# Kernel optimization log

Hardware: AMD Instinct MI355X
Metric: run time of the kernel (lower is better)

The kernel has to match this reference:

```python
import math
import jax, jax.numpy as jnp
import numpy as np

B, T, C, H = 2, 2048, 1024, 16
MAX_SEQ = 2048


def _make_pe(max_seq: int, dim: int, base: float = 10000.0) -> np.ndarray:
    pe = np.zeros((max_seq, dim), dtype=np.float32)
    position = np.arange(max_seq, dtype=np.float32)[:, None]
    div_term = np.exp(np.arange(0, dim, 2, dtype=np.float32) * (-math.log(base) / dim))
    pe[:, 0::2] = np.sin(position * div_term)
    pe[:, 1::2] = np.cos(position * div_term)
    return pe


def setup_inputs() -> dict:
    key = jax.random.key(0)
    k1, k2, k3 = jax.random.split(key, 3)
    x = jax.random.normal(k1, (B, T, C), dtype=jnp.float32)
    # torch Linear default init scale ~ 1/sqrt(fan_in)
    w_qkv = jax.random.normal(k2, (3 * C, C), dtype=jnp.float32) / math.sqrt(C)
    w_proj = jax.random.normal(k3, (C, C), dtype=jnp.float32) / math.sqrt(C)
    pe = jnp.asarray(_make_pe(MAX_SEQ, C))
    return {"x": x, "w_qkv": w_qkv, "w_proj": w_proj, "pe": pe}


def reference(x, w_qkv, w_proj, pe):
    b, t, c = x.shape
    h = H
    d = c // h
    # RoPE module adds sinusoidal PE under torch.no_grad() -> stop_gradient
    xp = jax.lax.stop_gradient(x + pe[None, :t, :])
    qkv = xp @ w_qkv.T  # [b, t, 3c]
    q, k, v = jnp.split(qkv, 3, axis=-1)
    q = q.reshape(b, t, h, d).transpose(0, 2, 1, 3)  # bhtd
    k = k.reshape(b, t, h, d).transpose(0, 2, 1, 3)
    v = v.reshape(b, t, h, d).transpose(0, 2, 1, 3)
    att = jnp.einsum("bhqd,bhkd->bhqk", q, k) * (1.0 / math.sqrt(d))
    causal = jnp.tril(jnp.ones((t, t), dtype=bool))  # [t, t]
    att = jnp.where(causal[None, None], att, -jnp.inf)
    att = jax.nn.softmax(att, axis=-1)
    y = jnp.einsum("bhqk,bhkd->bhqd", att, v)
    y = y.transpose(0, 2, 1, 3).reshape(b, t, c)
    return y @ w_proj.T
```

## Files before the change

kernel.cpp:

```cpp
#include <hip/hip_runtime.h>
#include <cstdint>

typedef __bf16 bf16x8 __attribute__((ext_vector_type(8)));
typedef __bf16 bf16x4 __attribute__((ext_vector_type(4)));
typedef float  f32x4  __attribute__((ext_vector_type(4)));

static constexpr int kB = 2, kT = 2048, kC = 1024, kH = 16, kD = 64;
static constexpr int kK = 1024;

__device__ __forceinline__ uint16_t f2bf(float f) {
  uint32_t u = __builtin_bit_cast(uint32_t, f);
  u += 0x7FFFu + ((u >> 16) & 1u);
  return (uint16_t)(u >> 16);
}

__device__ __forceinline__ void gl_lds16(const void* g, void* l) {
  __builtin_amdgcn_global_load_lds((__attribute__((address_space(1))) void*)(void*)g,
                                   (__attribute__((address_space(3))) void*)l, 16, 0, 0);
}

__global__ __launch_bounds__(256) void prep_xpe(const float* __restrict__ x,
                                                const float* __restrict__ pe,
                                                uint16_t* __restrict__ xp) {
  const int i = blockIdx.x * 256 + threadIdx.x;
  const float4 xv = ((const float4*)x)[i];
  const int c4 = i & (kC / 4 - 1);
  const int t = (i / (kC / 4)) & (kT - 1);
  const float4 pv = ((const float4*)pe)[t * (kC / 4) + c4];
  ushort4 o;
  o.x = f2bf(xv.x + pv.x);
  o.y = f2bf(xv.y + pv.y);
  o.z = f2bf(xv.z + pv.z);
  o.w = f2bf(xv.w + pv.w);
  ((ushort4*)xp)[i] = o;
}

__global__ __launch_bounds__(256) void cast_w(const float* __restrict__ w,
                                              uint16_t* __restrict__ o) {
  const int i = blockIdx.x * 256 + threadIdx.x;
  const float4 v = ((const float4*)w)[i];
  ushort4 u;
  u.x = f2bf(v.x); u.y = f2bf(v.y); u.z = f2bf(v.z); u.w = f2bf(v.w);
  ((ushort4*)o)[i] = u;
}

__global__ __launch_bounds__(512, 2) void gemm_qkv(const uint16_t* __restrict__ A,
                                                   const uint16_t* __restrict__ W,
                                                   uint16_t* __restrict__ qb,
                                                   uint16_t* __restrict__ kb,
                                                   uint16_t* __restrict__ vT) {
  __shared__ __align__(1024) char lds[131072];
  const int tid = threadIdx.x;
  const int lane = tid & 63;
  const int wid = tid >> 6;
  const int l15 = lane & 15, l4 = lane >> 4;
  const int WM = wid >> 2, WN = wid & 3;
  const int orig = (int)blockIdx.x;
  const int xcd = orig & 7, j = orig >> 3;
  const int m0 = (xcd * 2 + (j & 1)) * 256;
  const int n0 = (j >> 1) * 256;
  constexpr int NKT = kK / 64;
  constexpr int NIT = NKT / 2;

  f32x4 acc[4][4][2] = {};

  auto stage = [&](int isA, int buf, int half, int kt) {
#pragma unroll
    for (int c = 0; c < 2; ++c) {
      const int off = (c * 512 + tid) * 16;
      const int lr = off >> 7, cbl = off & 127;
      const size_t grow = (size_t)((isA ? m0 : n0) + half * 128 + lr) * kK + kt * 64;
      gl_lds16((const char*)(isA ? A : W) + grow * 2 + (cbl ^ ((lr & 7) << 4)),
               lds + (isA ? 0 : 65536) + buf * 32768 + half * 16384 + off);
    }
  };
  auto bar = [&] {
    asm volatile("" ::: "memory");
    __builtin_amdgcn_s_barrier();
    asm volatile("" ::: "memory");
  };

  stage(1, 0, 0, 0); stage(0, 0, 0, 0);
  stage(1, 0, 1, 0); stage(0, 0, 1, 0);
  stage(1, 1, 0, 1); stage(0, 1, 0, 1);

  for (int i = 0; i < NIT; ++i) {
#pragma unroll
    for (int p = 0; p < 8; ++p) {
      constexpr int ISA[8] = {1, 0, 1, 0, 1, 0, 1, 0};
      constexpr int HLF[8] = {1, 1, 0, 0, 1, 1, 0, 0};
      constexpr int TOF[8] = {1, 1, 2, 2, 2, 2, 3, 3};
      const int qr = (p >> 1) & 1, qc = p & 1;
      const int cbuf = (p >> 2) & 1, q4 = p & 3;
      {
        int kt = 2 * i + TOF[p];
        if (kt > NKT - 1) kt = NKT - 1;
        stage(ISA[p], TOF[p] & 1, HLF[p], kt);
      }
      const char* Ab = lds + cbuf * 32768 + qr * 16384;
      const char* Bb = lds + 65536 + cbuf * 32768 + qc * 16384;
      bf16x8 af[2][4], bfr[2][2];
      auto reads = [&] {
#pragma unroll
        for (int ks = 0; ks < 2; ++ks) {
#pragma unroll
          for (int mt = 0; mt < 4; ++mt) {
            const int lr = WM * 64 + mt * 16 + l15;
            af[ks][mt] = *(const bf16x8*)(Ab + lr * 128 +
                                          ((ks * 64 + l4 * 16) ^ ((lr & 7) << 4)));
          }
#pragma unroll
          for (int nt = 0; nt < 2; ++nt) {
            const int lr = WN * 32 + nt * 16 + l15;
            bfr[ks][nt] = *(const bf16x8*)(Bb + lr * 128 +
                                           ((ks * 64 + l4 * 16) ^ ((lr & 7) << 4)));
          }
        }
      };
      if (p == 0 || p == 4) {
        asm volatile("s_waitcnt vmcnt(6)" ::: "memory");
        bar();
        reads();
      } else {
        reads();
        bar();
      }
      __builtin_amdgcn_s_setprio(1);
#pragma unroll
      for (int ks = 0; ks < 2; ++ks)
#pragma unroll
        for (int mt = 0; mt < 4; ++mt)
#pragma unroll
          for (int nt = 0; nt < 2; ++nt)
            acc[q4][mt][nt] = __builtin_amdgcn_mfma_f32_16x16x32_bf16(
                af[ks][mt], bfr[ks][nt], acc[q4][mt][nt], 0, 0, 0);
      __builtin_amdgcn_s_setprio(0);
      bar();
    }
  }
  asm volatile("s_waitcnt vmcnt(0)" ::: "memory");
  bar();

  const int sec = n0 >> 10;
  const int b = m0 >> 11, tb = m0 & (kT - 1);
  if (sec < 2) {
    uint16_t* dst = (sec == 0) ? qb : kb;
#pragma unroll
    for (int q4 = 0; q4 < 4; ++q4) {
      const int qr = q4 >> 1, qc = q4 & 1;
#pragma unroll
      for (int mt = 0; mt < 4; ++mt)
#pragma unroll
        for (int nt = 0; nt < 2; ++nt)
#pragma unroll
          for (int r = 0; r < 4; ++r) {
            const int m = qr * 128 + WM * 64 + mt * 16 + l4 * 4 + r;
            const int nn = (n0 & (kC - 1)) + qc * 128 + WN * 32 + nt * 16 + l15;
            const int h = nn >> 6, d = nn & 63;
            dst[((size_t)((b * kH + h) * kT + tb + m)) * kD + d] =
                f2bf(acc[q4][mt][nt][r]);
          }
    }
  } else {
#pragma unroll
    for (int q4 = 0; q4 < 4; ++q4) {
      const int qr = q4 >> 1, qc = q4 & 1;
#pragma unroll
      for (int mt = 0; mt < 4; ++mt)
#pragma unroll
        for (int nt = 0; nt < 2; ++nt) {
          const int nl = qc * 128 + WN * 32 + nt * 16 + l15;
          const int mb2 = (qr * 128 + WM * 64 + mt * 16 + l4 * 4) * 2;
          ushort4 pk;
          pk.x = f2bf(acc[q4][mt][nt][0]);
          pk.y = f2bf(acc[q4][mt][nt][1]);
          pk.z = f2bf(acc[q4][mt][nt][2]);
          pk.w = f2bf(acc[q4][mt][nt][3]);
          *(ushort4*)(lds + nl * 512 + (mb2 ^ ((nl & 7) << 4))) = pk;
        }
    }
    bar();
#pragma unroll
    for (int it = 0; it < 16; ++it) {
      const int chunk = it * 512 + tid;
      const int nr = chunk >> 5, mb = (chunk & 31) * 16;
      const bf16x8 v = *(const bf16x8*)(lds + nr * 512 + (mb ^ ((nr & 7) << 4)));
      const int nn = (n0 - 2048) + nr;
      const int h = nn >> 6, d = nn & 63;
      *(bf16x8*)(vT + ((size_t)((b * kH + h) * kD + d)) * kT + tb + (chunk & 31) * 8) = v;
    }
  }
}

__global__ __launch_bounds__(256) void gemm_proj(const uint16_t* __restrict__ A,
                                                 const uint16_t* __restrict__ W,
                                                 float* __restrict__ out) {
  __shared__ __align__(1024) char lds[32768];
  const int lane = threadIdx.x & 63;
  const int wid = threadIdx.x >> 6;
  const int l15 = lane & 15, l4 = lane >> 4;
  const int wm = wid >> 1, wn = wid & 1;
  const int orig = (int)(blockIdx.y * gridDim.x + blockIdx.x);
  const int xcd = orig & 7, j = orig >> 3;
  const int m0 = (xcd * 4 + (j & 3)) * 128;
  const int n0 = (j >> 2) * 128;

  f32x4 acc[4][4] = {};

  for (int k0 = 0; k0 < kK; k0 += 64) {
#pragma unroll
    for (int jj = 0; jj < 4; ++jj) {
      const int off = wid * 4096 + jj * 1024 + lane * 16;
      const int row = off >> 7;
      const int colb = (off & 127) ^ ((row & 7) << 4);
      gl_lds16((const char*)A + ((size_t)(m0 + row) * kK + k0) * 2 + colb,
               lds + wid * 4096 + jj * 1024);
      gl_lds16((const char*)W + ((size_t)(n0 + row) * kK + k0) * 2 + colb,
               lds + 16384 + wid * 4096 + jj * 1024);
    }
    __syncthreads();
#pragma unroll
    for (int ks = 0; ks < 2; ++ks) {
      bf16x8 af[4], bf_[4];
#pragma unroll
      for (int mt = 0; mt < 4; ++mt) {
        const int r = wm * 64 + mt * 16 + l15;
        const int cb = (l4 * 16 + ks * 64) ^ ((r & 7) << 4);
        af[mt] = *(const bf16x8*)(lds + r * 128 + cb);
      }
#pragma unroll
      for (int nt = 0; nt < 4; ++nt) {
        const int r = wn * 64 + nt * 16 + l15;
        const int cb = (l4 * 16 + ks * 64) ^ ((r & 7) << 4);
        bf_[nt] = *(const bf16x8*)(lds + 16384 + r * 128 + cb);
      }
#pragma unroll
      for (int mt = 0; mt < 4; ++mt)
#pragma unroll
        for (int nt = 0; nt < 4; ++nt)
          acc[mt][nt] = __builtin_amdgcn_mfma_f32_16x16x32_bf16(af[mt], bf_[nt],
                                                                acc[mt][nt], 0, 0, 0);
    }
    __syncthreads();
  }

#pragma unroll
  for (int mt = 0; mt < 4; ++mt)
#pragma unroll
    for (int nt = 0; nt < 4; ++nt)
#pragma unroll
      for (int r = 0; r < 4; ++r) {
        const int m = m0 + wm * 64 + mt * 16 + l4 * 4 + r;
        const int n = n0 + wn * 64 + nt * 16 + l15;
        out[(size_t)m * kC + n] = acc[mt][nt][r];
      }
}

__global__ __launch_bounds__(256, 4) void attn(const uint16_t* __restrict__ qb,
                                               const uint16_t* __restrict__ kb,
                                               const uint16_t* __restrict__ vT,
                                               uint16_t* __restrict__ y) {
  __shared__ __align__(1024) char lds[40960];
  const int lane = threadIdx.x & 63;
  const int wid = threadIdx.x >> 6;
  const int l15 = lane & 15, l4 = lane >> 4;
  const int bh = blockIdx.x;
  const int qt = (int)(gridDim.y - 1) - (int)blockIdx.y;
  const int q0 = qt * 64 + wid * 16;
  const size_t base = (size_t)bh * kT * kD;
  const uint16_t* Q = qb + base;
  const uint16_t* Kp = kb + base;
  const uint16_t* Vt = vT + base;
  char* P = lds + 32768 + wid * 2048;
  const int xr = (l15 & 7) << 4;

  bf16x8 qf[2];
#pragma unroll
  for (int ks = 0; ks < 2; ++ks) {
    bf16x8 t = *(const bf16x8*)(Q + (size_t)(q0 + l15) * kD + ks * 32 + l4 * 8);
#pragma unroll
    for (int i = 0; i < 8; ++i) t[i] = (__bf16)((float)t[i] * 0.1803368801f);
    qf[ks] = t;
  }

  float m_ = -1e30f, l_ = 0.f;
  f32x4 o[4];
#pragma unroll
  for (int nt = 0; nt < 4; ++nt) o[nt] = (f32x4){0.f, 0.f, 0.f, 0.f};

  const int nkt = qt + 1;

  auto STAGE = [&](int bi, int k0) {
#pragma unroll
    for (int c = 0; c < 2; ++c) {
      const int call = wid * 2 + c;
      const int row = call * 8 + (lane >> 3);
      const int colb = (((lane & 7) ^ ((lane >> 3) & 7)) << 4);
      gl_lds16((const char*)Kp + ((size_t)(k0 + row) * kD) * 2 + colb,
               lds + bi * 8192 + call * 1024);
      gl_lds16((const char*)Vt + ((size_t)row * kT + k0) * 2 + colb,
               lds + 16384 + bi * 8192 + call * 1024);
    }
  };

  int cur = 0;
  STAGE(0, 0);
  for (int kt = 0; kt < nkt; ++kt) {
    const int k0 = kt * 64;
    const bool hasnext = (kt + 1 < nkt);
    if (hasnext) STAGE(cur ^ 1, k0 + 64);
    if (hasnext)
      asm volatile("s_waitcnt vmcnt(4)" ::: "memory");
    else
      asm volatile("s_waitcnt vmcnt(0)" ::: "memory");
    __builtin_amdgcn_s_barrier();
    asm volatile("" ::: "memory");

    const char* Kb = lds + cur * 8192;
    const char* Vb = lds + 16384 + cur * 8192;

    f32x4 s[4] = {};
    __builtin_amdgcn_s_setprio(1);
#pragma unroll
    for (int ks = 0; ks < 2; ++ks)
#pragma unroll
      for (int nt = 0; nt < 4; ++nt) {
        const bf16x8 kf =
            *(const bf16x8*)(Kb + (nt * 16 + l15) * 128 + ((ks * 64 + l4 * 16) ^ xr));
        s[nt] = __builtin_amdgcn_mfma_f32_16x16x32_bf16(kf, qf[ks], s[nt], 0, 0, 0);
      }
    __builtin_amdgcn_s_setprio(0);

    if (kt == nkt - 1) {
      const int qq = q0 + l15;
#pragma unroll
      for (int nt = 0; nt < 4; ++nt)
#pragma unroll
        for (int r = 0; r < 4; ++r)
          if (k0 + nt * 16 + l4 * 4 + r > qq) s[nt][r] = -1e30f;
    }

    float pm = s[0][0];
#pragma unroll
    for (int nt = 0; nt < 4; ++nt)
#pragma unroll
      for (int r = 0; r < 4; ++r) pm = fmaxf(pm, s[nt][r]);
    if (!__all(pm <= m_ + 11.0f)) {
      float rm = fmaxf(pm, __shfl_xor(pm, 16));
      rm = fmaxf(rm, __shfl_xor(rm, 32));
      const float newm = fmaxf(m_, rm);
      const float sc = exp2f(m_ - newm);
      m_ = newm;
      l_ *= sc;
#pragma unroll
      for (int nt = 0; nt < 4; ++nt)
#pragma unroll
        for (int r = 0; r < 4; ++r) o[nt][r] *= sc;
    }
    float ps = 0.f;
#pragma unroll
    for (int nt = 0; nt < 4; ++nt)
#pragma unroll
      for (int r = 0; r < 4; ++r) {
        const float p = exp2f(s[nt][r] - m_);
        s[nt][r] = p;
        ps += p;
      }
    l_ += ps;

#pragma unroll
    for (int nt = 0; nt < 4; ++nt) {
      bf16x4 pk;
#pragma unroll
      for (int r = 0; r < 4; ++r) pk[r] = (__bf16)s[nt][r];
      *(bf16x4*)(P + l15 * 128 + ((nt * 32 + l4 * 8) ^ xr)) = pk;
    }
    asm volatile("s_waitcnt lgkmcnt(0)" ::: "memory");
    __builtin_amdgcn_sched_barrier(0);

    bf16x8 pf[2];
#pragma unroll
    for (int ks = 0; ks < 2; ++ks)
      pf[ks] = *(const bf16x8*)(P + l15 * 128 + ((ks * 64 + l4 * 16) ^ xr));
    __builtin_amdgcn_s_setprio(1);
#pragma unroll
    for (int ks = 0; ks < 2; ++ks)
#pragma unroll
      for (int nt = 0; nt < 4; ++nt) {
        const bf16x8 vf =
            *(const bf16x8*)(Vb + (nt * 16 + l15) * 128 + ((ks * 64 + l4 * 16) ^ xr));
        o[nt] = __builtin_amdgcn_mfma_f32_16x16x32_bf16(vf, pf[ks], o[nt], 0, 0, 0);
      }
    __builtin_amdgcn_s_setprio(0);

    __builtin_amdgcn_s_barrier();
    asm volatile("" ::: "memory");
    cur ^= 1;
  }

  l_ += __shfl_xor(l_, 16);
  l_ += __shfl_xor(l_, 32);
  const float inv = 1.0f / l_;
  const int b = bh >> 4, h = bh & 15;
  const int q = q0 + l15;
#pragma unroll
  for (int nt = 0; nt < 4; ++nt) {
    bf16x4 yv;
#pragma unroll
    for (int r = 0; r < 4; ++r) yv[r] = (__bf16)(o[nt][r] * inv);
    *(bf16x4*)(y + ((size_t)(b * kT + q)) * kC + h * kD + nt * 16 + l4 * 4) = yv;
  }
}

extern "C" void kernel_launch(void* const* d_in, const int* in_sizes, int n_in,
                              void* d_out, int out_size, void* d_ws, size_t ws_size,
                              hipStream_t stream) {
  const float* x = (const float*)d_in[0];
  const float* wqkv = (const float*)d_in[1];
  const float* wproj = (const float*)d_in[2];
  const float* pe = (const float*)d_in[3];

  char* ws = (char*)d_ws;
  uint16_t* xp = (uint16_t*)(ws);
  uint16_t* wq = (uint16_t*)(ws + (size_t)(8u << 20));
  uint16_t* wp = (uint16_t*)(ws + (size_t)(14u << 20));
  uint16_t* qbuf = (uint16_t*)(ws + (size_t)(16u << 20));
  uint16_t* kbuf = (uint16_t*)(ws + (size_t)(24u << 20));
  uint16_t* vTb = (uint16_t*)(ws + (size_t)(32u << 20));

  prep_xpe<<<dim3(kB * kT * kC / 4 / 256), 256, 0, stream>>>(x, pe, xp);
  cast_w<<<dim3(3 * kC * kC / 4 / 256), 256, 0, stream>>>(wqkv, wq);
  cast_w<<<dim3(kC * kC / 4 / 256), 256, 0, stream>>>(wproj, wp);

  gemm_qkv<<<dim3(192), 512, 0, stream>>>(xp, wq, qbuf, kbuf, vTb);

  attn<<<dim3(kB * kH, kT / 64), 256, 0, stream>>>(qbuf, kbuf, vTb, xp);

  gemm_proj<<<dim3(32, 8), 256, 0, stream>>>(xp, wp, (float*)d_out);
}
```

Measured before the change: 113.6 us.

## Fuse prep kernels and give each attention wave two query tiles

Merges the x+pe cast and the two weight-cast kernels into one launch. The attention kernel now runs 2 waves per block, each handling 32 query rows as two 16-row tiles, so every K and V fragment read from LDS feeds two MFMAs. The softmax now starts the score accumulator at -m so it can skip the max subtraction, and it rescales only when the running max grows by more than a threshold. This trades fewer waves per block and more registers per wave for less LDS traffic per MFMA and fewer kernel launches.

After: 127.7 us. +12.3%, slower.

```diff
diff --git a/kernel.cpp b/kernel.cpp
--- a/kernel.cpp
+++ b/kernel.cpp
@@ -19,29 +19,40 @@
                                    (__attribute__((address_space(3))) void*)l, 16, 0, 0);
 }
 
-__global__ __launch_bounds__(256) void prep_xpe(const float* __restrict__ x,
+__global__ __launch_bounds__(256) void prep_all(const float* __restrict__ x,
                                                 const float* __restrict__ pe,
-                                                uint16_t* __restrict__ xp) {
+                                                const float* __restrict__ wqkv,
+                                                const float* __restrict__ wproj,
+                                                uint16_t* __restrict__ xp,
+                                                uint16_t* __restrict__ wq,
+                                                uint16_t* __restrict__ wp) {
+  constexpr int NX = kB * kT * kC / 4;
+  constexpr int NWQ = 3 * kC * kC / 4;
   const int i = blockIdx.x * 256 + threadIdx.x;
-  const float4 xv = ((const float4*)x)[i];
-  const int c4 = i & (kC / 4 - 1);
-  const int t = (i / (kC / 4)) & (kT - 1);
-  const float4 pv = ((const float4*)pe)[t * (kC / 4) + c4];
-  ushort4 o;
-  o.x = f2bf(xv.x + pv.x);
-  o.y = f2bf(xv.y + pv.y);
-  o.z = f2bf(xv.z + pv.z);
-  o.w = f2bf(xv.w + pv.w);
-  ((ushort4*)xp)[i] = o;
-}
-
-__global__ __launch_bounds__(256) void cast_w(const float* __restrict__ w,
-                                              uint16_t* __restrict__ o) {
-  const int i = blockIdx.x * 256 + threadIdx.x;
-  const float4 v = ((const float4*)w)[i];
-  ushort4 u;
-  u.x = f2bf(v.x); u.y = f2bf(v.y); u.z = f2bf(v.z); u.w = f2bf(v.w);
-  ((ushort4*)o)[i] = u;
+  if (i < NX) {
+    const float4 xv = ((const float4*)x)[i];
+    const int c4 = i & (kC / 4 - 1);
+    const int t = (i / (kC / 4)) & (kT - 1);
+    const float4 pv = ((const float4*)pe)[t * (kC / 4) + c4];
+    ushort4 o;
+    o.x = f2bf(xv.x + pv.x);
+    o.y = f2bf(xv.y + pv.y);
+    o.z = f2bf(xv.z + pv.z);
+    o.w = f2bf(xv.w + pv.w);
+    ((ushort4*)xp)[i] = o;
+  } else if (i < NX + NWQ) {
+    const int j = i - NX;
+    const float4 v = ((const float4*)wqkv)[j];
+    ushort4 u;
+    u.x = f2bf(v.x); u.y = f2bf(v.y); u.z = f2bf(v.z); u.w = f2bf(v.w);
+    ((ushort4*)wq)[j] = u;
+  } else {
+    const int j = i - NX - NWQ;
+    const float4 v = ((const float4*)wproj)[j];
+    ushort4 u;
+    u.x = f2bf(v.x); u.y = f2bf(v.y); u.z = f2bf(v.z); u.w = f2bf(v.w);
+    ((ushort4*)wp)[j] = u;
+  }
 }
 
 __global__ __launch_bounds__(512, 2) void gemm_qkv(const uint16_t* __restrict__ A,
@@ -256,7 +267,7 @@
       }
 }
 
-__global__ __launch_bounds__(256, 4) void attn(const uint16_t* __restrict__ qb,
+__global__ __launch_bounds__(128, 2) void attn(const uint16_t* __restrict__ qb,
                                                const uint16_t* __restrict__ kb,
                                                const uint16_t* __restrict__ vT,
                                                uint16_t* __restrict__ y) {
@@ -266,34 +277,35 @@
   const int l15 = lane & 15, l4 = lane >> 4;
   const int bh = blockIdx.x;
   const int qt = (int)(gridDim.y - 1) - (int)blockIdx.y;
-  const int q0 = qt * 64 + wid * 16;
+  const int q0w = qt * 64 + wid * 32;
   const size_t base = (size_t)bh * kT * kD;
   const uint16_t* Q = qb + base;
   const uint16_t* Kp = kb + base;
   const uint16_t* Vt = vT + base;
-  char* P = lds + 32768 + wid * 2048;
+  char* P = lds + 32768 + wid * 4096;
   const int xr = (l15 & 7) << 4;
 
-  bf16x8 qf[2];
-#pragma unroll
-  for (int ks = 0; ks < 2; ++ks) {
-    bf16x8 t = *(const bf16x8*)(Q + (size_t)(q0 + l15) * kD + ks * 32 + l4 * 8);
-#pragma unroll
-    for (int i = 0; i < 8; ++i) t[i] = (__bf16)((float)t[i] * 0.1803368801f);
-    qf[ks] = t;
-  }
-
-  float m_ = -1e30f, l_ = 0.f;
-  f32x4 o[4];
-#pragma unroll
-  for (int nt = 0; nt < 4; ++nt) o[nt] = (f32x4){0.f, 0.f, 0.f, 0.f};
+  bf16x8 qf[2][2];
+#pragma unroll
+  for (int h = 0; h < 2; ++h)
+#pragma unroll
+    for (int ks = 0; ks < 2; ++ks) {
+      bf16x8 t =
+          *(const bf16x8*)(Q + (size_t)(q0w + h * 16 + l15) * kD + ks * 32 + l4 * 8);
+#pragma unroll
+      for (int i = 0; i < 8; ++i) t[i] = (__bf16)((float)t[i] * 0.1803368801f);
+      qf[h][ks] = t;
+    }
+
+  float m_[2] = {0.f, 0.f}, l_[2] = {0.f, 0.f};
+  f32x4 o[2][4] = {};
 
   const int nkt = qt + 1;
 
   auto STAGE = [&](int bi, int k0) {
 #pragma unroll
-    for (int c = 0; c < 2; ++c) {
-      const int call = wid * 2 + c;
+    for (int c = 0; c < 4; ++c) {
+      const int call = wid * 4 + c;
       const int row = call * 8 + (lane >> 3);
       const int colb = (((lane & 7) ^ ((lane >> 3) & 7)) << 4);
       gl_lds16((const char*)Kp + ((size_t)(k0 + row) * kD) * 2 + colb,
@@ -310,7 +322,7 @@
     const bool hasnext = (kt + 1 < nkt);
     if (hasnext) STAGE(cur ^ 1, k0 + 64);
     if (hasnext)
-      asm volatile("s_waitcnt vmcnt(4)" ::: "memory");
+      asm volatile("s_waitcnt vmcnt(8)" ::: "memory");
     else
       asm volatile("s_waitcnt vmcnt(0)" ::: "memory");
     __builtin_amdgcn_s_barrier();
@@ -319,7 +331,12 @@
     const char* Kb = lds + cur * 8192;
     const char* Vb = lds + 16384 + cur * 8192;
 
-    f32x4 s[4] = {};
+    f32x4 s[2][4];
+#pragma unroll
+    for (int h = 0; h < 2; ++h)
+#pragma unroll
+      for (int nt = 0; nt < 4; ++nt)
+        s[h][nt] = (f32x4){-m_[h], -m_[h], -m_[h], -m_[h]};
     __builtin_amdgcn_s_setprio(1);
 #pragma unroll
     for (int ks = 0; ks < 2; ++ks)
@@ -327,61 +344,76 @@
       for (int nt = 0; nt < 4; ++nt) {
         const bf16x8 kf =
             *(const bf16x8*)(Kb + (nt * 16 + l15) * 128 + ((ks * 64 + l4 * 16) ^ xr));
-        s[nt] = __builtin_amdgcn_mfma_f32_16x16x32_bf16(kf, qf[ks], s[nt], 0, 0, 0);
+        s[0][nt] = __builtin_amdgcn_mfma_f32_16x16x32_bf16(kf, qf[0][ks], s[0][nt], 0, 0, 0);
+        s[1][nt] = __builtin_amdgcn_mfma_f32_16x16x32_bf16(kf, qf[1][ks], s[1][nt], 0, 0, 0);
       }
     __builtin_amdgcn_s_setprio(0);
 
-    if (kt == nkt - 1) {
-      const int qq = q0 + l15;
+#pragma unroll
+    for (int h = 0; h < 2; ++h) {
+      if (k0 + 63 > q0w + h * 16) {
+        const int qq = q0w + h * 16 + l15;
+#pragma unroll
+        for (int nt = 0; nt < 4; ++nt)
+#pragma unroll
+          for (int r = 0; r < 4; ++r)
+            if (k0 + nt * 16 + l4 * 4 + r > qq) s[h][nt][r] = -1e30f;
+      }
+      float pm = s[h][0][0];
 #pragma unroll
       for (int nt = 0; nt < 4; ++nt)
 #pragma unroll
-        for (int r = 0; r < 4; ++r)
-          if (k0 + nt * 16 + l4 * 4 + r > qq) s[nt][r] = -1e30f;
-    }
-
-    float pm = s[0][0];
-#pragma unroll
-    for (int nt = 0; nt < 4; ++nt)
-#pragma unroll
-      for (int r = 0; r < 4; ++r) pm = fmaxf(pm, s[nt][r]);
-    if (!__all(pm <= m_ + 11.0f)) {
-      float rm = fmaxf(pm, __shfl_xor(pm, 16));
-      rm = fmaxf(rm, __shfl_xor(rm, 32));
-      const float newm = fmaxf(m_, rm);
-      const float sc = exp2f(m_ - newm);
-      m_ = newm;
-      l_ *= sc;
-#pragma unroll
-      for (int nt = 0; nt < 4; ++nt)
-#pragma unroll
-        for (int r = 0; r < 4; ++r) o[nt][r] *= sc;
-    }
-    float ps = 0.f;
-#pragma unroll
-    for (int nt = 0; nt < 4; ++nt)
-#pragma unroll
-      for (int r = 0; r < 4; ++r) {
-        const float p = exp2f(s[nt][r] - m_);
-        s[nt][r] = p;
-        ps += p;
-      }
-    l_ += ps;
-
-#pragma unroll
-    for (int nt = 0; nt < 4; ++nt) {
-      bf16x4 pk;
-#pragma unroll
-      for (int r = 0; r < 4; ++r) pk[r] = (__bf16)s[nt][r];
-      *(bf16x4*)(P + l15 * 128 + ((nt * 32 + l4 * 8) ^ xr)) = pk;
+        for (int r = 0; r < 4; ++r) pm = fmaxf(pm, s[h][nt][r]);
+      float ps = 0.f;
+      if (__all(pm <= 11.0f)) {
+#pragma unroll
+        for (int nt = 0; nt < 4; ++nt)
+#pragma unroll
+          for (int r = 0; r < 4; ++r) {
+            const float p = exp2f(s[h][nt][r]);
+            s[h][nt][r] = p;
+            ps += p;
+          }
+      } else {
+        float rm = fmaxf(pm, __shfl_xor(pm, 16));
+        rm = fmaxf(rm, __shfl_xor(rm, 32));
+        const float rmc = fmaxf(rm, 0.f);
+        const float sc = exp2f(-rmc);
+        m_[h] += rmc;
+        l_[h] *= sc;
+#pragma unroll
+        for (int nt = 0; nt < 4; ++nt)
+#pragma unroll
+          for (int r = 0; r < 4; ++r) o[h][nt][r] *= sc;
+#pragma unroll
+        for (int nt = 0; nt < 4; ++nt)
+#pragma unroll
+          for (int r = 0; r < 4; ++r) {
+            const float p = exp2f(s[h][nt][r] - rmc);
+            s[h][nt][r] = p;
+            ps += p;
+          }
+      }
+      l_[h] += ps;
+
+#pragma unroll
+      for (int nt = 0; nt < 4; ++nt) {
+        bf16x4 pk;
+#pragma unroll
+        for (int r = 0; r < 4; ++r) pk[r] = (__bf16)s[h][nt][r];
+        *(bf16x4*)(P + h * 2048 + l15 * 128 + ((nt * 32 + l4 * 8) ^ xr)) = pk;
+      }
     }
     asm volatile("s_waitcnt lgkmcnt(0)" ::: "memory");
     __builtin_amdgcn_sched_barrier(0);
 
-    bf16x8 pf[2];
-#pragma unroll
-    for (int ks = 0; ks < 2; ++ks)
-      pf[ks] = *(const bf16x8*)(P + l15 * 128 + ((ks * 64 + l4 * 16) ^ xr));
+    bf16x8 pf[2][2];
+#pragma unroll
+    for (int h = 0; h < 2; ++h)
+#pragma unroll
+      for (int ks = 0; ks < 2; ++ks)
+        pf[h][ks] =
+            *(const bf16x8*)(P + h * 2048 + l15 * 128 + ((ks * 64 + l4 * 16) ^ xr));
     __builtin_amdgcn_s_setprio(1);
 #pragma unroll
     for (int ks = 0; ks < 2; ++ks)
@@ -389,7 +421,8 @@
       for (int nt = 0; nt < 4; ++nt) {
         const bf16x8 vf =
             *(const bf16x8*)(Vb + (nt * 16 + l15) * 128 + ((ks * 64 + l4 * 16) ^ xr));
-        o[nt] = __builtin_amdgcn_mfma_f32_16x16x32_bf16(vf, pf[ks], o[nt], 0, 0, 0);
+        o[0][nt] = __builtin_amdgcn_mfma_f32_16x16x32_bf16(vf, pf[0][ks], o[0][nt], 0, 0, 0);
+        o[1][nt] = __builtin_amdgcn_mfma_f32_16x16x32_bf16(vf, pf[1][ks], o[1][nt], 0, 0, 0);
       }
     __builtin_amdgcn_s_setprio(0);
 
@@ -398,17 +431,20 @@
     cur ^= 1;
   }
 
-  l_ += __shfl_xor(l_, 16);
-  l_ += __shfl_xor(l_, 32);
-  const float inv = 1.0f / l_;
-  const int b = bh >> 4, h = bh & 15;
-  const int q = q0 + l15;
-#pragma unroll
-  for (int nt = 0; nt < 4; ++nt) {
-    bf16x4 yv;
-#pragma unroll
-    for (int r = 0; r < 4; ++r) yv[r] = (__bf16)(o[nt][r] * inv);
-    *(bf16x4*)(y + ((size_t)(b * kT + q)) * kC + h * kD + nt * 16 + l4 * 4) = yv;
+  const int b = bh >> 4, h16 = bh & 15;
+#pragma unroll
+  for (int h = 0; h < 2; ++h) {
+    float lsum = l_[h] + __shfl_xor(l_[h], 16);
+    lsum += __shfl_xor(lsum, 32);
+    const float inv = 1.0f / lsum;
+    const int q = q0w + h * 16 + l15;
+#pragma unroll
+    for (int nt = 0; nt < 4; ++nt) {
+      bf16x4 yv;
+#pragma unroll
+      for (int r = 0; r < 4; ++r) yv[r] = (__bf16)(o[h][nt][r] * inv);
+      *(bf16x4*)(y + ((size_t)(b * kT + q)) * kC + h16 * kD + nt * 16 + l4 * 4) = yv;
+    }
   }
 }
 
@@ -428,13 +464,11 @@
   uint16_t* kbuf = (uint16_t*)(ws + (size_t)(24u << 20));
   uint16_t* vTb = (uint16_t*)(ws + (size_t)(32u << 20));
 
-  prep_xpe<<<dim3(kB * kT * kC / 4 / 256), 256, 0, stream>>>(x, pe, xp);
-  cast_w<<<dim3(3 * kC * kC / 4 / 256), 256, 0, stream>>>(wqkv, wq);
-  cast_w<<<dim3(kC * kC / 4 / 256), 256, 0, stream>>>(wproj, wp);
+  prep_all<<<dim3(8192), 256, 0, stream>>>(x, pe, wqkv, wproj, xp, wq, wp);
 
   gemm_qkv<<<dim3(192), 512, 0, stream>>>(xp, wq, qbuf, kbuf, vTb);
 
-  attn<<<dim3(kB * kH, kT / 64), 256, 0, stream>>>(qbuf, kbuf, vTb, xp);
+  attn<<<dim3(kB * kH, kT / 64), 128, 0, stream>>>(qbuf, kbuf, vTb, xp);
 
   gemm_proj<<<dim3(32, 8), 256, 0, stream>>>(xp, wp, (float*)d_out);
 }
```
